# Optimization experiments

Hardware: AMD Instinct MI355X
Metric: run time of the kernel (lower is better)

## Reference

```python
import jax, jax.numpy as jnp
import numpy as np

NEG_SLOPE = 0.01  # nn.LeakyReLU default

def leaky(x):
    return jnp.where(x >= 0, x, NEG_SLOPE * x)

def setup_inputs() -> dict:
    key = jax.random.key(0)
    ks = jax.random.split(key, 10)
    N, E, IN_DIM, OUT_DIM = 100000, 1600000, 128, 128
    indices = jax.random.randint(ks[0], (2, E), 0, N, dtype=jnp.int64 if jax.config.jax_enable_x64 else jnp.int32)
    features = jax.random.normal(ks[1], (N, IN_DIM), dtype=jnp.float32)
    s = 1.0 / np.sqrt(IN_DIM)
    W_att_w = jax.random.uniform(ks[2], (OUT_DIM, IN_DIM), minval=-s, maxval=s)
    W_att_b = jax.random.uniform(ks[3], (OUT_DIM,), minval=-s, maxval=s)
    W1_w = jax.random.uniform(ks[4], (OUT_DIM, IN_DIM), minval=-s, maxval=s)
    W1_b = jax.random.uniform(ks[5], (OUT_DIM,), minval=-s, maxval=s)
    W2_w = jax.random.uniform(ks[6], (OUT_DIM, OUT_DIM), minval=-s, maxval=s)
    W2_b = jax.random.uniform(ks[7], (OUT_DIM,), minval=-s, maxval=s)
    # xavier_uniform for a: gain*sqrt(6/(fan_in+fan_out)), fan_in=2*OUT_DIM, fan_out=1
    lim = float(np.sqrt(6.0 / (2 * OUT_DIM + 1)))
    a = jax.random.uniform(ks[8], (2 * OUT_DIM, 1), minval=-lim, maxval=lim)
    return {"indices": indices, "features": features, "num_nodes": N,
            "W_att_w": W_att_w, "W_att_b": W_att_b, "W1_w": W1_w, "W1_b": W1_b,
            "W2_w": W2_w, "W2_b": W2_b, "a": a}

def reference(indices, features, num_nodes, W_att_w, W_att_b, W1_w, W1_b, W2_w, W2_b, a):
    src, dst = indices[0], indices[1]
    out_dim = W_att_w.shape[0]
    # h_trans = W_att(features)
    h_trans = features @ W_att_w.T + W_att_b  # [N, D]
    # cat([src_h, dst_h]) @ a  ==  src_h @ a[:D] + dst_h @ a[D:]  (avoids materializing cat)
    a_src, a_dst = a[:out_dim], a[out_dim:]
    logits = leaky(h_trans[src] @ a_src + h_trans[dst] @ a_dst)  # [E, 1]
    # edge softmax over incoming edges of each dst (raw exp, as in original)
    exp_l = jnp.exp(logits)
    denom = jax.ops.segment_sum(exp_l, dst, num_segments=num_nodes)  # [N, 1]
    alpha = exp_l / (denom[dst] + 1e-9)  # [E, 1]
    # sparse.mm(adj_att, W1(features)) == segment_sum of alpha * msg[src] over dst
    h_msg = features @ W1_w.T + W1_b  # [N, D]
    h_neigh = jax.ops.segment_sum(alpha * h_msg[src], dst, num_segments=num_nodes)  # [N, D]
    h_self = features  # in_dim == out_dim branch
    term1 = h_self + h_neigh
    term2 = (h_self * h_neigh) @ W2_w.T + W2_b
    return leaky(term1 + term2)
```

## Files before the change

kernel.cpp:

```cpp
#include <hip/hip_runtime.h>

#define D 128
typedef __attribute__((ext_vector_type(8))) short short8;
typedef __attribute__((ext_vector_type(4))) float f32x4;

__device__ __forceinline__ float leaky(float x){ return x >= 0.f ? x : 0.01f*x; }
__device__ __forceinline__ unsigned short f2bf(float x){
    unsigned u = __float_as_uint(x);
    u = (u + 0x7fffu + ((u>>16)&1u)) >> 16;
    return (unsigned short)u;
}
__device__ __forceinline__ short8 pack8m(f32x4 a, f32x4 b){
    short8 s;
    s[0]=(short)f2bf(a[0]); s[1]=(short)f2bf(a[1]);
    s[2]=(short)f2bf(a[2]); s[3]=(short)f2bf(a[3]);
    s[4]=(short)f2bf(b[0]); s[5]=(short)f2bf(b[1]);
    s[6]=(short)f2bf(b[2]); s[7]=(short)f2bf(b[3]);
    return s;
}

__global__ void k_prep(const float* __restrict__ Ww, const float* __restrict__ Wb,
                       const float* __restrict__ a, float* __restrict__ v,
                       const float* __restrict__ W1, const float* __restrict__ W2,
                       unsigned short* __restrict__ W1b, unsigned short* __restrict__ W2b){
    int b = blockIdx.x;
    if(b < 64){
        int i = b*256 + threadIdx.x;
        W1b[i] = f2bf(W1[i]);
        W2b[i] = f2bf(W2[i]);
        return;
    }
    int i = threadIdx.x; if(i >= 128) return;
    float vs=0.f, vd=0.f;
    for (int o=0;o<D;++o){ float w = Ww[o*D+i]; vs = fmaf(w, a[o], vs); vd = fmaf(w, a[D+o], vd); }
    v[i]=vs; v[D+i]=vd;
    if(i==0){
        float cs=0.f,cd=0.f;
        for(int o=0;o<D;++o){ cs=fmaf(Wb[o],a[o],cs); cd=fmaf(Wb[o],a[D+o],cd); }
        v[256]=cs; v[257]=cd;
    }
}

__global__ __launch_bounds__(256) void k_msgscal(const float* __restrict__ F,
        const unsigned short* __restrict__ W1b, const float* __restrict__ b1,
        const float* __restrict__ v, unsigned short* __restrict__ Hp,
        float* __restrict__ ss, float* __restrict__ sd, int N,
        const int* __restrict__ dst, unsigned* __restrict__ M,
        int E, int GT, int CHUNK, int NB){
    __shared__ __align__(16) unsigned short Wlds[17408];
    if((int)blockIdx.x >= GT){
        unsigned* h = (unsigned*)Wlds;
        for(int i=threadIdx.x;i<NB;i+=256) h[i]=0u;
        __syncthreads();
        int blk = (int)blockIdx.x - GT;
        int s = blk*CHUNK;
        int e = s+CHUNK < E ? s+CHUNK : E;
        for(int i=s+(int)threadIdx.x;i<e;i+=256) atomicAdd(&h[((unsigned)dst[i])>>6],1u);
        __syncthreads();
        for(int j=threadIdx.x;j<NB;j+=256) M[(size_t)j*256 + blk] = h[j];
        return;
    }
    #pragma unroll
    for(int k=0;k<8;++k){
        int idx = ((int)threadIdx.x + k*256)*8;
        int row = idx >> 7, col = idx & 127;
        *(short8*)(&Wlds[row*136 + col]) = *(const short8*)(W1b + idx);
    }
    __syncthreads();
    const int lane = threadIdx.x & 63, wv = threadIdx.x>>6;
    const int t = lane & 15, g = lane >> 4;
    float bb[8];
    #pragma unroll
    for(int j=0;j<8;++j) bb[j] = b1[j*16+t];
    const float c_s = v[256], c_d = v[257];
    const int Mt = (N+15)>>4;
    for(int rt = (int)blockIdx.x*4 + wv; rt < Mt; rt += GT*4){
        int row0 = rt*16 + t;
        int row = row0 < N ? row0 : N-1;
        const float* fr = F + (size_t)row*D + g*8;
        f32x4 acc[8];
        #pragma unroll
        for(int j=0;j<8;++j) acc[j] = (f32x4){0.f,0.f,0.f,0.f};
        float ds = 0.f, dd = 0.f;
        #pragma unroll
        for(int kk=0;kk<4;++kk){
            f32x4 lo = *(const f32x4*)(fr + kk*32);
            f32x4 hi = *(const f32x4*)(fr + kk*32 + 4);
            f32x4 vsl = *(const f32x4*)(v + kk*32 + g*8);
            f32x4 vsh = *(const f32x4*)(v + kk*32 + g*8 + 4);
            f32x4 vdl = *(const f32x4*)(v + D + kk*32 + g*8);
            f32x4 vdh = *(const f32x4*)(v + D + kk*32 + g*8 + 4);
            #pragma unroll
            for(int q=0;q<4;++q){
                ds = fmaf(lo[q], vsl[q], ds); ds = fmaf(hi[q], vsh[q], ds);
                dd = fmaf(lo[q], vdl[q], dd); dd = fmaf(hi[q], vdh[q], dd);
            }
            short8 af = pack8m(lo, hi);
            #pragma unroll
            for(int j=0;j<8;++j){
                short8 wfj = *(const short8*)(&Wlds[(j*16+t)*136 + kk*32 + g*8]);
                acc[j] = __builtin_amdgcn_mfma_f32_16x16x32_bf16(af, wfj, acc[j], 0,0,0);
            }
        }
        ds += __shfl_xor(ds,16); ds += __shfl_xor(ds,32);
        dd += __shfl_xor(dd,16); dd += __shfl_xor(dd,32);
        if(g==0 && row0 < N){ ss[row0] = ds + c_s; sd[row0] = dd + c_d; }
        #pragma unroll
        for(int r=0;r<4;++r){
            int rr = rt*16 + g*4 + r;
            if(rr < N){
                short8 h;
                #pragma unroll
                for(int j=0;j<8;++j) h[j] = (short)f2bf(acc[j][r] + bb[j]);
                *(short8*)(Hp + (size_t)rr*D + t*8) = h;
            }
        }
    }
}

__global__ __launch_bounds__(256) void k_scanA(const unsigned* __restrict__ M,
        unsigned* __restrict__ bsum, int n){
    __shared__ unsigned lds[4];
    int base = blockIdx.x*4096 + threadIdx.x*16;
    unsigned s=0;
    #pragma unroll
    for(int k=0;k<16;++k){ int i=base+k; if(i<n) s+=M[i]; }
    #pragma unroll
    for(int o=1;o<64;o<<=1) s += __shfl_xor(s,o);
    if((threadIdx.x&63)==0) lds[threadIdx.x>>6]=s;
    __syncthreads();
    if(threadIdx.x==0) bsum[blockIdx.x] = lds[0]+lds[1]+lds[2]+lds[3];
}

__global__ __launch_bounds__(256) void k_scanC(const unsigned* __restrict__ M,
        const unsigned* __restrict__ bsum, unsigned* __restrict__ Msc, int n, int nsb){
    __shared__ unsigned lds[4];
    __shared__ unsigned ps[2];
    int t = threadIdx.x;
    unsigned pv = (t < nsb && t < (int)blockIdx.x) ? bsum[t] : 0u;
    #pragma unroll
    for(int o=1;o<64;o<<=1) pv += __shfl_xor(pv,o);
    if((t&63)==0 && t<128) ps[t>>6]=pv;
    int base = blockIdx.x*4096 + t*16;
    unsigned v[16]; unsigned tsum=0;
    #pragma unroll
    for(int k=0;k<16;++k){ int i=base+k; v[k]=(i<n)?M[i]:0u; tsum+=v[k]; }
    unsigned x=tsum;
    #pragma unroll
    for(int o=1;o<64;o<<=1){ unsigned y=__shfl_up(x,(unsigned)o); if((t&63)>=o) x+=y; }
    if((t&63)==63) lds[t>>6]=x;
    __syncthreads();
    unsigned run = ps[0]+ps[1];
    for(int w=0;w<(t>>6);++w) run += lds[w];
    run += (x - tsum);
    #pragma unroll
    for(int k=0;k<16;++k){ int i=base+k; if(i<n) Msc[i]=run; run+=v[k]; }
}

__global__ __launch_bounds__(256) void k_bscatter(const int* __restrict__ src,
        const int* __restrict__ dst, const unsigned* __restrict__ Msc,
        const float* __restrict__ ss, const float* __restrict__ sdv,
        uint2* __restrict__ ew, int E, int NB, int CHUNK){
    __shared__ unsigned hoff[1600];
    int blk = blockIdx.x, NBLKg = gridDim.x;
    for(int i=threadIdx.x;i<NB;i+=256) hoff[i] = Msc[(size_t)i*NBLKg + blk];
    __syncthreads();
    int s0 = blk*CHUNK;
    int e1 = s0+CHUNK < E ? s0+CHUNK : E;
    for(int i=s0+(int)threadIdx.x;i<e1;i+=256){
        int d = dst[i];
        int s = src[i];
        float w = __expf(leaky(ss[s] + sdv[d]));
        unsigned p = atomicAdd(&hoff[((unsigned)d)>>6], 1u);
        ew[p] = make_uint2(((unsigned)s<<6)|((unsigned)d&63u), __float_as_uint(w));
    }
}

__global__ __launch_bounds__(256) void k_fine(const uint2* __restrict__ ew,
        const unsigned* __restrict__ Msc, uint2* __restrict__ ewp,
        unsigned* __restrict__ offs, int N, int NB, int NBLKg, int E){
    __shared__ unsigned cA[64], cB[64], loff[64];
    __shared__ unsigned begS, endS;
    int b = blockIdx.x;
    int dbase = b<<6;
    if(threadIdx.x==0){
        begS = Msc[(size_t)b*NBLKg];
        endS = (b+1 < NB) ? Msc[(size_t)(b+1)*NBLKg] : (unsigned)E;
    }
    if(threadIdx.x<64){ cA[threadIdx.x]=0u; cB[threadIdx.x]=0u; }
    __syncthreads();
    const unsigned beg = begS, end = endS;
    for(unsigned i=beg+threadIdx.x; i<end; i+=256)
        atomicAdd(&cA[ew[i].x & 63u], 1u);
    __syncthreads();
    if(threadIdx.x<64){
        unsigned c = cA[threadIdx.x];
        unsigned x = c;
        #pragma unroll
        for(int o=1;o<64;o<<=1){ unsigned y = __shfl_up(x,(unsigned)o); if((int)threadIdx.x>=o) x += y; }
        loff[threadIdx.x] = x - c;
        int dd = dbase + (int)threadIdx.x;
        if(dd < N) offs[dd] = beg + x - c;
    }
    if(b==0 && threadIdx.x==64) offs[N] = (unsigned)E;
    if(b==0 && threadIdx.x>=80 && threadIdx.x<96)
        ewp[E + (threadIdx.x-80)] = make_uint2(0u, 0u);
    __syncthreads();
    for(unsigned i=beg+threadIdx.x; i<end; i+=256){
        uint2 p = ew[i];
        unsigned dl = p.x & 63u;
        unsigned r = atomicAdd(&cB[dl], 1u);
        ewp[beg + loff[dl] + r] = make_uint2(p.x >> 6, p.y);
    }
}

__device__ __forceinline__ void fma8(float* acc, uint4 u, float w){
    acc[0]=fmaf(w,__uint_as_float(u.x<<16),acc[0]);
    acc[1]=fmaf(w,__uint_as_float(u.x&0xffff0000u),acc[1]);
    acc[2]=fmaf(w,__uint_as_float(u.y<<16),acc[2]);
    acc[3]=fmaf(w,__uint_as_float(u.y&0xffff0000u),acc[3]);
    acc[4]=fmaf(w,__uint_as_float(u.z<<16),acc[4]);
    acc[5]=fmaf(w,__uint_as_float(u.z&0xffff0000u),acc[5]);
    acc[6]=fmaf(w,__uint_as_float(u.w<<16),acc[6]);
    acc[7]=fmaf(w,__uint_as_float(u.w&0xffff0000u),acc[7]);
}

__global__ __launch_bounds__(256) void k_gather(const unsigned* __restrict__ off,
        const uint2* __restrict__ ewp, const unsigned short* __restrict__ Hp,
        float* __restrict__ out, int N){
    const int wv = threadIdx.x>>6, l = threadIdx.x&63;
    const int d = blockIdx.x*4 + wv;
    if(d>=N) return;
    const int g = l>>4, t = l&15;
    const unsigned kb = off[d], ke = off[d+1];
    const unsigned toff = (unsigned)t*16u;
    float acc[8];
    #pragma unroll
    for(int j=0;j<8;++j) acc[j]=0.f;
    float den = 0.f;

    unsigned e = kb + g;
    uint2 p0 = ewp[e];
    uint4 u0 = *(const uint4*)((const char*)Hp + ((p0.x<<8) + toff));
    uint2 p1 = ewp[e+4];
    uint4 u1 = *(const uint4*)((const char*)Hp + ((p1.x<<8) + toff));
    while(e < ke){
        float w0 = __uint_as_float(p0.y);
        fma8(acc, u0, w0);
        p0 = ewp[e+8];
        u0 = *(const uint4*)((const char*)Hp + ((p0.x<<8) + toff));
        float w1 = (e+4 < ke) ? __uint_as_float(p1.y) : 0.f;
        fma8(acc, u1, w1);
        p1 = ewp[e+12];
        u1 = *(const uint4*)((const char*)Hp + ((p1.x<<8) + toff));
        den += w0 + w1;
        e += 8;
    }
    #pragma unroll
    for(int j=0;j<8;++j){
        acc[j] += __shfl_xor(acc[j],16);
        acc[j] += __shfl_xor(acc[j],32);
    }
    den += __shfl_xor(den,16);
    den += __shfl_xor(den,32);
    float inv = 1.f/(den + 1e-9f);
    int c = g*32 + t;
    out[(size_t)d*D + c]      = acc[g*2]  * inv;
    out[(size_t)d*D + c + 16] = acc[g*2+1]* inv;
}

__global__ __launch_bounds__(256) void k_final(const float* __restrict__ F,
        const unsigned short* __restrict__ W2b, const float* __restrict__ b2,
        float* __restrict__ out, int N, int GF){
    __shared__ __align__(16) unsigned short Wlds[17408];
    #pragma unroll
    for(int k=0;k<8;++k){
        int idx = ((int)threadIdx.x + k*256)*8;
        int row = idx >> 7, col = idx & 127;
        *(short8*)(&Wlds[row*136 + col]) = *(const short8*)(W2b + idx);
    }
    __syncthreads();
    const int lane = threadIdx.x & 63, wv = threadIdx.x>>6;
    const int t = lane & 15, g = lane >> 4;
    float bb[8];
    #pragma unroll
    for(int j=0;j<8;++j) bb[j] = b2[j*16+t];
    const int Mt = (N+15)>>4;
    for(int rt = (int)blockIdx.x*4 + wv; rt < Mt; rt += GF*4){
        int row = rt*16 + t; if(row>=N) row = N-1;
        const float* fr = F   + (size_t)row*D + g*8;
        const float* hr = out + (size_t)row*D + g*8;
        f32x4 acc[8];
        #pragma unroll
        for(int j=0;j<8;++j) acc[j] = (f32x4){0.f,0.f,0.f,0.f};
        #pragma unroll
        for(int kk=0;kk<4;++kk){
            f32x4 flo = *(const f32x4*)(fr + kk*32);
            f32x4 fhi = *(const f32x4*)(fr + kk*32 + 4);
            f32x4 hlo = *(const f32x4*)(hr + kk*32);
            f32x4 hhi = *(const f32x4*)(hr + kk*32 + 4);
            short8 af = pack8m(flo*hlo, fhi*hhi);
            #pragma unroll
            for(int j=0;j<8;++j){
                short8 wfj = *(const short8*)(&Wlds[(j*16+t)*136 + kk*32 + g*8]);
                acc[j] = __builtin_amdgcn_mfma_f32_16x16x32_bf16(af, wfj, acc[j], 0,0,0);
            }
        }
        #pragma unroll
        for(int r=0;r<4;++r){
            int rr = rt*16 + g*4 + r;
            if(rr < N){
                #pragma unroll
                for(int j=0;j<8;++j){
                    int c = j*16 + t;
                    float f = F[(size_t)rr*D + c];
                    float h = out[(size_t)rr*D + c];
                    out[(size_t)rr*D + c] = leaky(f + h + acc[j][r] + bb[j]);
                }
            }
        }
    }
}

extern "C" void kernel_launch(void* const* d_in, const int* in_sizes, int n_in,
                              void* d_out, int out_size, void* d_ws, size_t ws_size,
                              hipStream_t stream) {
    const int*   idx  = (const int*)  d_in[0];
    const float* F    = (const float*)d_in[1];
    const float* Waw  = (const float*)d_in[3];
    const float* Wab  = (const float*)d_in[4];
    const float* W1w  = (const float*)d_in[5];
    const float* W1b  = (const float*)d_in[6];
    const float* W2w  = (const float*)d_in[7];
    const float* W2b  = (const float*)d_in[8];
    const float* a    = (const float*)d_in[9];
    float* out = (float*)d_out;

    const int E = in_sizes[0]/2;
    const int N = in_sizes[1]/D;
    const int* srcp = idx;
    const int* dstp = idx + E;

    const int NBLK = 256;
    const int CHUNK = (E + NBLK - 1)/NBLK;
    const int NB = (N + 63)/64;
    const int NT = NB*NBLK;
    const int NSB = (NT + 4095)/4096;

    uint2*    ew   = (uint2*)d_ws;
    uint2*    ewp  = ew + E;
    unsigned short* Hp  = (unsigned short*)(ewp + E + 16);
    unsigned short* W1c = Hp + (size_t)N*D;
    unsigned short* W2c = W1c + 16384;
    float*    ss   = (float*)(W2c + 16384);
    float*    sd   = ss + N;
    float*    v    = sd + N;
    unsigned* M    = (unsigned*)(v + 320);
    unsigned* Msc  = M + NT;
    unsigned* bsum = Msc + NT + 2;
    unsigned* offs = bsum + NSB + 2;

    const int Mt = (N+15)/16;
    const int GT = (Mt+3)/4;
    const int GF = GT;

    k_prep    <<<65, 256, 0, stream>>>(Waw, Wab, a, v, W1w, W2w, W1c, W2c);
    k_msgscal <<<GT+NBLK, 256, 0, stream>>>(F, W1c, W1b, v, Hp, ss, sd, N,
                                            dstp, M, E, GT, CHUNK, NB);
    k_scanA   <<<NSB, 256, 0, stream>>>(M, bsum, NT);
    k_scanC   <<<NSB, 256, 0, stream>>>(M, bsum, Msc, NT, NSB);
    k_bscatter<<<NBLK, 256, 0, stream>>>(srcp, dstp, Msc, ss, sd, ew, E, NB, CHUNK);
    k_fine    <<<NB, 256, 0, stream>>>(ew, Msc, ewp, offs, N, NB, NBLK, E);
    k_gather  <<<(N+3)/4, 256, 0, stream>>>(offs, ewp, Hp, out, N);
    k_final   <<<GF, 256, 0, stream>>>(F, W2c, W2b, out, N, GF);
}
```

Before: 192.9 us.

## Fuse fine bucket sort into gather using shared-memory edge staging

Merges the per-bucket fine sort and the neighbor gather into a single kernel. Each block sorts its 64-destination bucket's edges into LDS and then gathers directly, so the sorted edge array and offsets no longer make a round trip through global memory, and one launch is dropped. Buckets with more edges than CAP fall back to a slow path that rescans the bucket once per destination. The grid shrinks from N/4 blocks to N/64 blocks, and the roughly 20KB of LDS per block may limit occupancy for the latency-bound gather.

```diff
diff --git a/kernel.cpp b/kernel.cpp
--- a/kernel.cpp
+++ b/kernel.cpp
@@ -1,6 +1,7 @@
 #include <hip/hip_runtime.h>
 
 #define D 128
+#define CAP 2560
 typedef __attribute__((ext_vector_type(8))) short short8;
 typedef __attribute__((ext_vector_type(4))) float f32x4;
 
@@ -176,44 +177,6 @@
     }
 }
 
-__global__ __launch_bounds__(256) void k_fine(const uint2* __restrict__ ew,
-        const unsigned* __restrict__ Msc, uint2* __restrict__ ewp,
-        unsigned* __restrict__ offs, int N, int NB, int NBLKg, int E){
-    __shared__ unsigned cA[64], cB[64], loff[64];
-    __shared__ unsigned begS, endS;
-    int b = blockIdx.x;
-    int dbase = b<<6;
-    if(threadIdx.x==0){
-        begS = Msc[(size_t)b*NBLKg];
-        endS = (b+1 < NB) ? Msc[(size_t)(b+1)*NBLKg] : (unsigned)E;
-    }
-    if(threadIdx.x<64){ cA[threadIdx.x]=0u; cB[threadIdx.x]=0u; }
-    __syncthreads();
-    const unsigned beg = begS, end = endS;
-    for(unsigned i=beg+threadIdx.x; i<end; i+=256)
-        atomicAdd(&cA[ew[i].x & 63u], 1u);
-    __syncthreads();
-    if(threadIdx.x<64){
-        unsigned c = cA[threadIdx.x];
-        unsigned x = c;
-        #pragma unroll
-        for(int o=1;o<64;o<<=1){ unsigned y = __shfl_up(x,(unsigned)o); if((int)threadIdx.x>=o) x += y; }
-        loff[threadIdx.x] = x - c;
-        int dd = dbase + (int)threadIdx.x;
-        if(dd < N) offs[dd] = beg + x - c;
-    }
-    if(b==0 && threadIdx.x==64) offs[N] = (unsigned)E;
-    if(b==0 && threadIdx.x>=80 && threadIdx.x<96)
-        ewp[E + (threadIdx.x-80)] = make_uint2(0u, 0u);
-    __syncthreads();
-    for(unsigned i=beg+threadIdx.x; i<end; i+=256){
-        uint2 p = ew[i];
-        unsigned dl = p.x & 63u;
-        unsigned r = atomicAdd(&cB[dl], 1u);
-        ewp[beg + loff[dl] + r] = make_uint2(p.x >> 6, p.y);
-    }
-}
-
 __device__ __forceinline__ void fma8(float* acc, uint4 u, float w){
     acc[0]=fmaf(w,__uint_as_float(u.x<<16),acc[0]);
     acc[1]=fmaf(w,__uint_as_float(u.x&0xffff0000u),acc[1]);
@@ -225,48 +188,117 @@
     acc[7]=fmaf(w,__uint_as_float(u.w&0xffff0000u),acc[7]);
 }
 
-__global__ __launch_bounds__(256) void k_gather(const unsigned* __restrict__ off,
-        const uint2* __restrict__ ewp, const unsigned short* __restrict__ Hp,
-        float* __restrict__ out, int N){
-    const int wv = threadIdx.x>>6, l = threadIdx.x&63;
-    const int d = blockIdx.x*4 + wv;
-    if(d>=N) return;
+__global__ __launch_bounds__(256) void k_gfine(const uint2* __restrict__ ew,
+        const unsigned* __restrict__ Msc, const unsigned short* __restrict__ Hp,
+        float* __restrict__ out, int N, int NB, int E){
+    __shared__ uint2 sed[CAP+16];
+    __shared__ unsigned cA[64], cB[64], loff[64];
+    __shared__ unsigned begS, endS;
+    const int b = blockIdx.x;
+    const int dbase = b<<6;
+    const int tid = threadIdx.x;
+    if(tid==0){
+        begS = Msc[(size_t)b*256];
+        endS = (b+1 < NB) ? Msc[(size_t)(b+1)*256] : (unsigned)E;
+    }
+    if(tid<64){ cA[tid]=0u; cB[tid]=0u; }
+    __syncthreads();
+    const unsigned beg = begS;
+    const unsigned size = endS - begS;
+    const int wv = tid>>6, l = tid&63;
     const int g = l>>4, t = l&15;
-    const unsigned kb = off[d], ke = off[d+1];
     const unsigned toff = (unsigned)t*16u;
-    float acc[8];
-    #pragma unroll
-    for(int j=0;j<8;++j) acc[j]=0.f;
-    float den = 0.f;
-
-    unsigned e = kb + g;
-    uint2 p0 = ewp[e];
-    uint4 u0 = *(const uint4*)((const char*)Hp + ((p0.x<<8) + toff));
-    uint2 p1 = ewp[e+4];
-    uint4 u1 = *(const uint4*)((const char*)Hp + ((p1.x<<8) + toff));
-    while(e < ke){
-        float w0 = __uint_as_float(p0.y);
-        fma8(acc, u0, w0);
-        p0 = ewp[e+8];
-        u0 = *(const uint4*)((const char*)Hp + ((p0.x<<8) + toff));
-        float w1 = (e+4 < ke) ? __uint_as_float(p1.y) : 0.f;
-        fma8(acc, u1, w1);
-        p1 = ewp[e+12];
-        u1 = *(const uint4*)((const char*)Hp + ((p1.x<<8) + toff));
-        den += w0 + w1;
-        e += 8;
-    }
-    #pragma unroll
-    for(int j=0;j<8;++j){
-        acc[j] += __shfl_xor(acc[j],16);
-        acc[j] += __shfl_xor(acc[j],32);
-    }
-    den += __shfl_xor(den,16);
-    den += __shfl_xor(den,32);
-    float inv = 1.f/(den + 1e-9f);
-    int c = g*32 + t;
-    out[(size_t)d*D + c]      = acc[g*2]  * inv;
-    out[(size_t)d*D + c + 16] = acc[g*2+1]* inv;
+
+    if(size <= CAP){
+        for(unsigned i=tid; i<size; i+=256)
+            atomicAdd(&cA[ew[beg+i].x & 63u], 1u);
+        __syncthreads();
+        if(tid<64){
+            unsigned c = cA[tid];
+            unsigned x = c;
+            #pragma unroll
+            for(int o=1;o<64;o<<=1){ unsigned y = __shfl_up(x,(unsigned)o); if(tid>=o) x += y; }
+            loff[tid] = x - c;
+        }
+        __syncthreads();
+        for(unsigned i=tid; i<size; i+=256){
+            uint2 p = ew[beg+i];
+            unsigned dl = p.x & 63u;
+            unsigned r = atomicAdd(&cB[dl], 1u);
+            sed[loff[dl]+r] = make_uint2(p.x>>6, p.y);
+        }
+        for(unsigned i=size+tid; i<size+16u; i+=256) sed[i] = make_uint2(0u,0u);
+        __syncthreads();
+        #pragma unroll 1
+        for(int i=0;i<16;++i){
+            int dl = i*4 + wv;
+            int d = dbase + dl;
+            if(d >= N) continue;
+            unsigned kb = loff[dl], ke = kb + cB[dl];
+            float acc[8];
+            #pragma unroll
+            for(int j=0;j<8;++j) acc[j]=0.f;
+            float den = 0.f;
+            unsigned e = kb + g;
+            uint2 p0 = sed[e];
+            uint4 u0 = *(const uint4*)((const char*)Hp + ((p0.x<<8) + toff));
+            uint2 p1 = sed[e+4];
+            uint4 u1 = *(const uint4*)((const char*)Hp + ((p1.x<<8) + toff));
+            while(e < ke){
+                float w0 = __uint_as_float(p0.y);
+                fma8(acc, u0, w0);
+                p0 = sed[e+8];
+                u0 = *(const uint4*)((const char*)Hp + ((p0.x<<8) + toff));
+                float w1 = (e+4 < ke) ? __uint_as_float(p1.y) : 0.f;
+                fma8(acc, u1, w1);
+                p1 = sed[e+12];
+                u1 = *(const uint4*)((const char*)Hp + ((p1.x<<8) + toff));
+                den += w0 + w1;
+                e += 8;
+            }
+            #pragma unroll
+            for(int j=0;j<8;++j){
+                acc[j] += __shfl_xor(acc[j],16);
+                acc[j] += __shfl_xor(acc[j],32);
+            }
+            den += __shfl_xor(den,16);
+            den += __shfl_xor(den,32);
+            float inv = 1.f/(den + 1e-9f);
+            int c = g*32 + t;
+            out[(size_t)d*D + c]      = acc[g*2]  * inv;
+            out[(size_t)d*D + c + 16] = acc[g*2+1]* inv;
+        }
+    } else {
+        #pragma unroll 1
+        for(int i=0;i<16;++i){
+            int dl = i*4 + wv;
+            int d = dbase + dl;
+            if(d >= N) continue;
+            float acc[8];
+            #pragma unroll
+            for(int j=0;j<8;++j) acc[j]=0.f;
+            float den = 0.f;
+            for(unsigned e2 = beg + (unsigned)g; e2 < beg + size; e2 += 4){
+                uint2 p = ew[e2];
+                if((int)(p.x & 63u) != dl) continue;
+                float w = __uint_as_float(p.y);
+                uint4 u = *(const uint4*)((const char*)Hp + (((p.x>>6)<<8) + toff));
+                fma8(acc, u, w);
+                den += w;
+            }
+            #pragma unroll
+            for(int j=0;j<8;++j){
+                acc[j] += __shfl_xor(acc[j],16);
+                acc[j] += __shfl_xor(acc[j],32);
+            }
+            den += __shfl_xor(den,16);
+            den += __shfl_xor(den,32);
+            float inv = 1.f/(den + 1e-9f);
+            int c = g*32 + t;
+            out[(size_t)d*D + c]      = acc[g*2]  * inv;
+            out[(size_t)d*D + c + 16] = acc[g*2+1]* inv;
+        }
+    }
 }
 
 __global__ __launch_bounds__(256) void k_final(const float* __restrict__ F,
@@ -348,8 +380,7 @@
     const int NSB = (NT + 4095)/4096;
 
     uint2*    ew   = (uint2*)d_ws;
-    uint2*    ewp  = ew + E;
-    unsigned short* Hp  = (unsigned short*)(ewp + E + 16);
+    unsigned short* Hp  = (unsigned short*)(ew + E);
     unsigned short* W1c = Hp + (size_t)N*D;
     unsigned short* W2c = W1c + 16384;
     float*    ss   = (float*)(W2c + 16384);
@@ -358,7 +389,6 @@
     unsigned* M    = (unsigned*)(v + 320);
     unsigned* Msc  = M + NT;
     unsigned* bsum = Msc + NT + 2;
-    unsigned* offs = bsum + NSB + 2;
 
     const int Mt = (N+15)/16;
     const int GT = (Mt+3)/4;
@@ -370,7 +400,6 @@
     k_scanA   <<<NSB, 256, 0, stream>>>(M, bsum, NT);
     k_scanC   <<<NSB, 256, 0, stream>>>(M, bsum, Msc, NT, NSB);
     k_bscatter<<<NBLK, 256, 0, stream>>>(srcp, dstp, Msc, ss, sd, ew, E, NB, CHUNK);
-    k_fine    <<<NB, 256, 0, stream>>>(ew, Msc, ewp, offs, N, NB, NBLK, E);
-    k_gather  <<<(N+3)/4, 256, 0, stream>>>(offs, ewp, Hp, out, N);
+    k_gfine   <<<NB, 256, 0, stream>>>(ew, Msc, Hp, out, N, NB, E);
     k_final   <<<GF, 256, 0, stream>>>(F, W2c, W2b, out, N, GF);
 }
```

New measurement: 185.7 us. 1.04x faster.
